# Kernel optimization log

Measured on AMD Instinct MI355X. Metric: run time of the kernel, lower is better.

Reference implementation:

```python
import jax, jax.numpy as jnp
import numpy as np

N = 100000   # nodes
E = 1600000  # edges
D = 128      # feature dim (layers all 128)
G = 512      # graphs in batch
C = 10       # num_classes
EPS = 1e-5   # batchnorm eps


def setup_inputs() -> dict:
    key = jax.random.key(0)
    ks = jax.random.split(key, 16)
    s = 1.0 / np.sqrt(D)
    return {
        "x": jax.random.normal(ks[0], (N, D), jnp.float32),
        "edge_index": jax.random.randint(ks[1], (2, E), 0, N),
        "batch": jnp.sort(jax.random.randint(ks[2], (N,), 0, G)),
        "w1": jax.random.normal(ks[3], (D, D), jnp.float32) * s,
        "b1": jnp.zeros((D,), jnp.float32),
        "w2": jax.random.normal(ks[4], (D, D), jnp.float32) * s,
        "b2": jnp.zeros((D,), jnp.float32),
        "w3": jax.random.normal(ks[5], (D, D), jnp.float32) * s,
        "b3": jnp.zeros((D,), jnp.float32),
        "g1": jnp.ones((D,), jnp.float32),
        "be1": jnp.zeros((D,), jnp.float32),
        "g2": jnp.ones((D,), jnp.float32),
        "be2": jnp.zeros((D,), jnp.float32),
        "fc_w": jax.random.normal(ks[6], (D, C), jnp.float32) * s,
        "fc_b": jnp.zeros((C,), jnp.float32),
    }


def _gcn(x, src, dst, norm, W, b):
    # transform -> gather -> normalize -> scatter-add (PyG GCNConv)
    h = x @ W
    out = jax.ops.segment_sum(h[src] * norm[:, None], dst, num_segments=x.shape[0])
    return out + b


def _bn(x, g, b):
    # training-mode BatchNorm1d: batch mean / biased variance
    mu = jnp.mean(x, axis=0)
    var = jnp.mean((x - mu) ** 2, axis=0)
    return (x - mu) * jax.lax.rsqrt(var + EPS) * g + b


def reference(x, edge_index, batch, w1, b1, w2, b2, w3, b3, g1, be1, g2, be2, fc_w, fc_b):
    n = x.shape[0]
    loop = jnp.arange(n)
    src = jnp.concatenate([edge_index[0], loop])  # add self-loops
    dst = jnp.concatenate([edge_index[1], loop])
    deg = jax.ops.segment_sum(jnp.ones_like(src, x.dtype), dst, num_segments=n)
    dinv = jax.lax.rsqrt(jnp.maximum(deg, 1.0))  # deg >= 1 due to self-loops
    norm = dinv[src] * dinv[dst]  # symmetric normalization per edge

    h = jax.nn.relu(_gcn(x, src, dst, norm, w1, b1))        # conv1 + relu (bn1 unused, per source)
    h = jax.nn.relu(_gcn(h, src, dst, norm, w2, b2))        # conv2 + relu
    h = jax.nn.relu(_bn(h, g1, be1))                        # bn + relu
    h = jax.nn.relu(_gcn(h, src, dst, norm, w3, b3))        # conv3 + relu
    h = jax.nn.relu(_bn(h, g2, be2))                        # bn + relu

    cnt = jax.ops.segment_sum(jnp.ones((n,), h.dtype), batch, num_segments=G)
    pooled = jax.ops.segment_sum(h, batch, num_segments=G) / jnp.maximum(cnt, 1.0)[:, None]
    logits = pooled @ fc_w + fc_b
    return jax.nn.log_softmax(logits, axis=1)
```

## Files before the change

### kernel.cpp

```cpp
#include <hip/hip_runtime.h>
#include <hip/hip_bf16.h>
#include <math.h>

#define D 128
#define G_GRAPHS 512
#define C_CLASSES 10
#define BN_EPS 1e-5f
#define NBUCK_MAX 512
#define EDGE_CHUNK 4096
#define EPT 16
#define HIST_BLOCKS 512
#define BN_BLOCKS 512

typedef unsigned short u16;
typedef unsigned int u32;
typedef unsigned short ushort4_t __attribute__((ext_vector_type(4)));
typedef unsigned short ushort8_t __attribute__((ext_vector_type(8)));
typedef __bf16 bf16x8 __attribute__((ext_vector_type(8)));
typedef float floatx4 __attribute__((ext_vector_type(4)));
union B8 { ushort8_t u; bf16x8 b; };

__device__ __forceinline__ float bf_lo(u32 v) { return __uint_as_float(v << 16); }
__device__ __forceinline__ float bf_hi(u32 v) { return __uint_as_float(v & 0xffff0000u); }
__device__ __forceinline__ u16 f2bf(float f) {
    union { float f; u32 u; } x; x.f = f;
    u32 r = x.u + 0x7fff + ((x.u >> 16) & 1);
    return (u16)(r >> 16);
}
__device__ __forceinline__ u32 pack2bf(float a, float b) {
    return (u32)f2bf(a) | ((u32)f2bf(b) << 16);
}


__global__ __launch_bounds__(256) void bucket_hist_kernel(
    const int* __restrict__ dst, int* __restrict__ bucketCnt, int E, int nbuck,
    const int* __restrict__ batch, int* __restrict__ gstart, int N)
{
    int tid = threadIdx.x;
    if (blockIdx.x >= HIST_BLOCKS) {
        int i = (blockIdx.x - HIST_BLOCKS) * 256 + tid;
        if (i >= N) return;
        int b = batch[i];
        int prev = (i == 0) ? -1 : batch[i - 1];
        if (b != prev) {
            for (int g = prev + 1; g <= b; ++g) gstart[g] = i;
        }
        if (i == N - 1) {
            for (int g = b + 1; g <= G_GRAPHS; ++g) gstart[g] = N;
        }
        return;
    }
    __shared__ int h[NBUCK_MAX];
    for (int i = tid; i < NBUCK_MAX; i += 256) h[i] = 0;
    __syncthreads();
    for (int i = blockIdx.x * 256 + tid; i < E; i += HIST_BLOCKS * 256)
        atomicAdd(&h[dst[i] >> 8], 1);
    __syncthreads();
    for (int i = tid; i < nbuck; i += 256)
        if (h[i]) atomicAdd(&bucketCnt[i], h[i]);
}

__global__ void scan_buckets_kernel(
    const int* __restrict__ bucketCnt, int* __restrict__ bucketBase,
    int* __restrict__ bucketCursor, int* __restrict__ rowPtr, int nbuck, int N, int E)
{
    __shared__ int buf[2][512];
    int tid = threadIdx.x;
    int v = (tid < nbuck) ? bucketCnt[tid] : 0;
    buf[0][tid] = v;
    __syncthreads();
    int cur = 0;
    for (int off = 1; off < 512; off <<= 1) {
        buf[1 - cur][tid] = buf[cur][tid] + ((tid >= off) ? buf[cur][tid - off] : 0);
        cur ^= 1;
        __syncthreads();
    }
    if (tid < nbuck) {
        int b = buf[cur][tid] - v;
        bucketBase[tid] = b;
        bucketCursor[tid] = b;
    }
    if (tid == 0) { bucketBase[nbuck] = E; rowPtr[N] = E; }
}

__global__ __launch_bounds__(256) void scatter_pairs_kernel(
    const int* __restrict__ src, const int* __restrict__ dst,
    int* __restrict__ bucketCursor, u32* __restrict__ pairs, int E)
{
    __shared__ int h[NBUCK_MAX];
    __shared__ int base[NBUCK_MAX];
    int tid = threadIdx.x;
    int e0 = blockIdx.x * EDGE_CHUNK;
    for (int i = tid; i < NBUCK_MAX; i += 256) h[i] = 0;
    __syncthreads();
    int s[EPT], d[EPT], r[EPT];
#pragma unroll
    for (int j = 0; j < EPT; ++j) {
        int i = e0 + j * 256 + tid;
        if (i < E) {
            s[j] = src[i];
            d[j] = dst[i];
            r[j] = atomicAdd(&h[d[j] >> 8], 1);
        } else {
            d[j] = -1;
        }
    }
    __syncthreads();
    for (int i = tid; i < NBUCK_MAX; i += 256)
        if (h[i]) base[i] = atomicAdd(&bucketCursor[i], h[i]);
    __syncthreads();
#pragma unroll
    for (int j = 0; j < EPT; ++j) {
        if (d[j] >= 0) {
            int b = d[j] >> 8;
            pairs[base[b] + r[j]] = ((u32)s[j] << 8) | (u32)(d[j] & 255);
        }
    }
}

__global__ __launch_bounds__(256) void bucket_sort_kernel(
    const u32* __restrict__ pairs, const int* __restrict__ bucketBase,
    int* __restrict__ colIdx, int* __restrict__ rowPtr, float* __restrict__ dinv,
    int* __restrict__ degHist, int N)
{
    __shared__ int h[256];
    __shared__ int cur[256];
    __shared__ int sbuf[2][256];
    __shared__ int dh[16];
    int tid = threadIdx.x;
    int b = blockIdx.x;
    int s = bucketBase[b], e = bucketBase[b + 1];
    h[tid] = 0;
    if (tid < 16) dh[tid] = 0;
    __syncthreads();
    for (int i = s + tid; i < e; i += 256)
        atomicAdd(&h[pairs[i] & 255], 1);
    __syncthreads();
    int cnt = h[tid];
    sbuf[0][tid] = cnt;
    __syncthreads();
    int c = 0;
    for (int off = 1; off < 256; off <<= 1) {
        sbuf[1 - c][tid] = sbuf[c][tid] + ((tid >= off) ? sbuf[c][tid - off] : 0);
        c ^= 1;
        __syncthreads();
    }
    int excl = sbuf[c][tid] - cnt;
    int v = b * 256 + tid;
    if (v < N) {
        rowPtr[v] = s + excl;
        dinv[v] = rsqrtf((float)(cnt + 1));
        int key = (cnt + 15) >> 4;
        if (key > 15) key = 15;
        atomicAdd(&dh[key], 1);
    }
    cur[tid] = s + excl;
    __syncthreads();
    if (tid < 16 && dh[tid]) atomicAdd(&degHist[tid * 16], dh[tid]);
    for (int i = s + tid; i < e; i += 256) {
        u32 p = pairs[i];
        int pos = atomicAdd(&cur[p & 255], 1);
        colIdx[pos] = (int)(p >> 8);
    }
}

__global__ __launch_bounds__(256) void wconv_kernel(
    const float4* __restrict__ w1, const float4* __restrict__ w2,
    const float4* __restrict__ w3, u16* __restrict__ wtAll, u32* __restrict__ tzero,
    const int* __restrict__ degHist, int* __restrict__ degCursor)
{
    int tid = threadIdx.x;
    if (blockIdx.x == 3) {
        if (tid < 64) tzero[tid] = 0;
        return;
    }
    if (blockIdx.x == 4) {
        if (tid == 0) {
            int base = 0;
            for (int k = 15; k >= 0; --k) {
                degCursor[k * 16] = base;
                base += degHist[k * 16];
            }
        }
        return;
    }
    const float4* W = (blockIdx.x == 0) ? w1 : (blockIdx.x == 1) ? w2 : w3;
    u16* Wt = wtAll + (size_t)blockIdx.x * D * D;
#pragma unroll
    for (int i = 0; i < 16; ++i) {
        int idx = tid + i * 256;
        int k = idx >> 5, c4 = idx & 31;
        float4 v = W[idx];
        Wt[(4 * c4 + 0) * D + k] = f2bf(v.x);
        Wt[(4 * c4 + 1) * D + k] = f2bf(v.y);
        Wt[(4 * c4 + 2) * D + k] = f2bf(v.z);
        Wt[(4 * c4 + 3) * D + k] = f2bf(v.w);
    }
}

__global__ __launch_bounds__(256) void perm_scatter_kernel(
    const int* __restrict__ rowPtr, int* __restrict__ degCursor,
    int* __restrict__ perm, int N)
{
    __shared__ int lh[16], lbase[16];
    int tid = threadIdx.x;
    if (tid < 16) lh[tid] = 0;
    __syncthreads();
    int v = blockIdx.x * 256 + tid;
    int key = 0, r = 0;
    bool ok = (v < N);
    if (ok) {
        int deg = rowPtr[v + 1] - rowPtr[v];
        key = (deg + 15) >> 4;
        if (key > 15) key = 15;
        r = atomicAdd(&lh[key], 1);
    }
    __syncthreads();
    if (tid < 16 && lh[tid] > 0) lbase[tid] = atomicAdd(&degCursor[tid * 16], lh[tid]);
    __syncthreads();
    if (ok) perm[lbase[key] + r] = v;
}

#define XS_STRIDE 136
#define GEMM_GRID 768

__device__ __forceinline__ void gemm_core_and_store(
    const u16* Xs, const u16* Ws, const float* __restrict__ dinv,
    u16* __restrict__ Y, int row0, int nrows, int tid)
{
    int wid = tid >> 6, lane = tid & 63;
    int m = lane & 15, quad = lane >> 4;
    int xrow = wid * 16 + m;

    floatx4 acc[8] = {};
#pragma unroll
    for (int ks = 0; ks < 4; ++ks) {
        int kk = ks * 32 + quad * 8;
        B8 a;
        a.u = *(const ushort8_t*)&Xs[xrow * XS_STRIDE + kk];
#pragma unroll
        for (int t = 0; t < 8; ++t) {
            B8 b;
            b.u = *(const ushort8_t*)&Ws[(t * 16 + m) * XS_STRIDE + kk];
            acc[t] = __builtin_amdgcn_mfma_f32_16x16x32_bf16(b.b, a.b, acc[t], 0, 0, 0);
        }
    }
    int grow = row0 + xrow;
    if (grow < nrows) {
        float du = dinv[grow];
#pragma unroll
        for (int t = 0; t < 8; ++t) {
            ushort4_t o;
            o.x = f2bf(acc[t][0] * du); o.y = f2bf(acc[t][1] * du);
            o.z = f2bf(acc[t][2] * du); o.w = f2bf(acc[t][3] * du);
            *(ushort4_t*)&Y[(size_t)grow * D + t * 16 + quad * 4] = o;
        }
    }
}

__device__ __forceinline__ void stage_w(const u16* __restrict__ Wt, u16* Ws, int tid) {
    const ushort8_t* Wv = (const ushort8_t*)Wt;
#pragma unroll
    for (int i = 0; i < 8; ++i) {
        int idx = tid + i * 256;
        int n = idx >> 4, c8 = idx & 15;
        *(ushort8_t*)&Ws[n * XS_STRIDE + c8 * 8] = Wv[idx];
    }
}

__global__ __launch_bounds__(256) void gemm_mfma_f32in_kernel(
    const float4* __restrict__ X, const u16* __restrict__ Wt,
    const float* __restrict__ dinv, u16* __restrict__ Y, int nrows, int ntiles)
{
    __shared__ __align__(16) u16 Xs[64 * XS_STRIDE];
    __shared__ __align__(16) u16 Ws[128 * XS_STRIDE];
    int tid = threadIdx.x;
    stage_w(Wt, Ws, tid);
    for (int t = blockIdx.x; t < ntiles; t += gridDim.x) {
        int row0 = t * 64;
        __syncthreads();
#pragma unroll
        for (int i = 0; i < 8; ++i) {
            int idx = tid + i * 256;
            int r = idx >> 5, c4 = idx & 31;
            int gr = row0 + r;
            float4 v = make_float4(0.f, 0.f, 0.f, 0.f);
            if (gr < nrows) v = X[(size_t)gr * 32 + c4];
            ushort4_t o;
            o.x = f2bf(v.x); o.y = f2bf(v.y); o.z = f2bf(v.z); o.w = f2bf(v.w);
            *(ushort4_t*)&Xs[r * XS_STRIDE + c4 * 4] = o;
        }
        __syncthreads();
        gemm_core_and_store(Xs, Ws, dinv, Y, row0, nrows, tid);
    }
}

__global__ __launch_bounds__(256) void gemm_mfma_bf16in_kernel(
    const uint4* __restrict__ X, const u16* __restrict__ Wt,
    const float* __restrict__ gsum, const float* __restrict__ gsq,
    const float* __restrict__ gamma, const float* __restrict__ beta, float invN,
    const float* __restrict__ dinv, u16* __restrict__ Y, int nrows, int ntiles)
{
    __shared__ __align__(16) u16 Xs[64 * XS_STRIDE];
    __shared__ __align__(16) u16 Ws[128 * XS_STRIDE];
    __shared__ float scs[D], shs[D];
    int tid = threadIdx.x;
    bool fuse = (gsum != nullptr);
    stage_w(Wt, Ws, tid);
    if (fuse && tid < D) {
        float mu = gsum[tid] * invN;
        float var = gsq[tid] * invN - mu * mu;
        float sc = gamma[tid] * rsqrtf(var + BN_EPS);
        scs[tid] = sc;
        shs[tid] = beta[tid] - mu * sc;
    }
    for (int t = blockIdx.x; t < ntiles; t += gridDim.x) {
        int row0 = t * 64;
        __syncthreads();
#pragma unroll
        for (int i = 0; i < 4; ++i) {
            int idx = tid + i * 256;
            int r = idx >> 4, c8 = idx & 15;
            int gr = row0 + r;
            uint4 v = make_uint4(0, 0, 0, 0);
            if (gr < nrows) v = X[(size_t)gr * 16 + c8];
            if (fuse) {
                int k = c8 * 8;
                v.x = pack2bf(fmaxf(bf_lo(v.x) * scs[k]     + shs[k],     0.f),
                              fmaxf(bf_hi(v.x) * scs[k + 1] + shs[k + 1], 0.f));
                v.y = pack2bf(fmaxf(bf_lo(v.y) * scs[k + 2] + shs[k + 2], 0.f),
                              fmaxf(bf_hi(v.y) * scs[k + 3] + shs[k + 3], 0.f));
                v.z = pack2bf(fmaxf(bf_lo(v.z) * scs[k + 4] + shs[k + 4], 0.f),
                              fmaxf(bf_hi(v.z) * scs[k + 5] + shs[k + 5], 0.f));
                v.w = pack2bf(fmaxf(bf_lo(v.w) * scs[k + 6] + shs[k + 6], 0.f),
                              fmaxf(bf_hi(v.w) * scs[k + 7] + shs[k + 7], 0.f));
            }
            *(uint4*)&Xs[r * XS_STRIDE + c8 * 8] = v;
        }
        __syncthreads();
        gemm_core_and_store(Xs, Ws, dinv, Y, row0, nrows, tid);
    }
}

#define ACC8U(t)                                           \
    acc0 += bf_lo((t).x); acc1 += bf_hi((t).x);            \
    acc2 += bf_lo((t).y); acc3 += bf_hi((t).y);            \
    acc4 += bf_lo((t).z); acc5 += bf_hi((t).z);            \
    acc6 += bf_lo((t).w); acc7 += bf_hi((t).w);

#define IDX8(i, jj)                                        \
    i##0 = ci[(jj)];     i##1 = ci[(jj) + 1];              \
    i##2 = ci[(jj) + 2]; i##3 = ci[(jj) + 3];              \
    i##4 = ci[(jj) + 4]; i##5 = ci[(jj) + 5];              \
    i##6 = ci[(jj) + 6]; i##7 = ci[(jj) + 7];

#define OFF8(o, i, jj)                                     \
    o##0 = ((jj)     < len) ? ((u32)i##0 << 8) : zoff;     \
    o##1 = ((jj) + 1 < len) ? ((u32)i##1 << 8) : zoff;     \
    o##2 = ((jj) + 2 < len) ? ((u32)i##2 << 8) : zoff;     \
    o##3 = ((jj) + 3 < len) ? ((u32)i##3 << 8) : zoff;     \
    o##4 = ((jj) + 4 < len) ? ((u32)i##4 << 8) : zoff;     \
    o##5 = ((jj) + 5 < len) ? ((u32)i##5 << 8) : zoff;     \
    o##6 = ((jj) + 6 < len) ? ((u32)i##6 << 8) : zoff;     \
    o##7 = ((jj) + 7 < len) ? ((u32)i##7 << 8) : zoff;

#define GAT8(t, o)                                         \
    t##0 = *(const uint4*)(baseT + o##0);                  \
    t##1 = *(const uint4*)(baseT + o##1);                  \
    t##2 = *(const uint4*)(baseT + o##2);                  \
    t##3 = *(const uint4*)(baseT + o##3);                  \
    t##4 = *(const uint4*)(baseT + o##4);                  \
    t##5 = *(const uint4*)(baseT + o##5);                  \
    t##6 = *(const uint4*)(baseT + o##6);                  \
    t##7 = *(const uint4*)(baseT + o##7);

#define ACCC(t)                                            \
    ACC8U(t##0); ACC8U(t##1); ACC8U(t##2); ACC8U(t##3);    \
    ACC8U(t##4); ACC8U(t##5); ACC8U(t##6); ACC8U(t##7);

__global__ __launch_bounds__(256) void aggregate_kernel(
    const uint4* __restrict__ T, const int* __restrict__ colIdx,
    const int* __restrict__ rowPtr, const float* __restrict__ dinv,
    const float* __restrict__ bias, const int* __restrict__ perm,
    u32* __restrict__ outH, int n, u32 zoff)
{
    int tid = threadIdx.x;
    int fg = tid & 15;
    int grp = tid >> 4;
    int slot = blockIdx.x * 16 + grp;
    if (slot >= n) return;
    int row = perm[slot];

    const char* baseT = (const char*)T + fg * 16;

    uint4 sv = *(const uint4*)(baseT + ((size_t)(u32)row << 8));
    float acc0 = bf_lo(sv.x), acc1 = bf_hi(sv.x);
    float acc2 = bf_lo(sv.y), acc3 = bf_hi(sv.y);
    float acc4 = bf_lo(sv.z), acc5 = bf_hi(sv.z);
    float acc6 = bf_lo(sv.w), acc7 = bf_hi(sv.w);

    int s = rowPtr[row], e = rowPtr[row + 1];
    int len = e - s;
    const int* ci = colIdx + s;

    if (len > 0) {
        int npairs = (len + 15) >> 4;
        int ia0, ia1, ia2, ia3, ia4, ia5, ia6, ia7;
        int ib0, ib1, ib2, ib3, ib4, ib5, ib6, ib7;
        u32 oa0, oa1, oa2, oa3, oa4, oa5, oa6, oa7;
        u32 ob0, ob1, ob2, ob3, ob4, ob5, ob6, ob7;
        uint4 t0, t1, t2, t3, t4, t5, t6, t7;
        uint4 u0, u1, u2, u3, u4, u5, u6, u7;

        IDX8(ia, 0); IDX8(ib, 8);
        OFF8(oa, ia, 0);
        GAT8(t, oa);
        OFF8(ob, ib, 8);
        IDX8(ia, 16);
        GAT8(u, ob);

#pragma unroll 1
        for (int p = 1; p < npairs; ++p) {
            int j = p << 4;
            OFF8(oa, ia, j);
            IDX8(ib, j + 8);
            ACCC(t);
            GAT8(t, oa);
            OFF8(ob, ib, j + 8);
            ACCC(u);
            IDX8(ia, j + 16);
            GAT8(u, ob);
        }
        ACCC(t); ACCC(u);
    }

    float dr = dinv[row];
    const float2* bp = (const float2*)bias;
    float2 bq0 = bp[fg * 4 + 0];
    float2 bq1 = bp[fg * 4 + 1];
    float2 bq2 = bp[fg * 4 + 2];
    float2 bq3 = bp[fg * 4 + 3];
    uint4 o;
    o.x = pack2bf(fmaxf(dr * acc0 + bq0.x, 0.f), fmaxf(dr * acc1 + bq0.y, 0.f));
    o.y = pack2bf(fmaxf(dr * acc2 + bq1.x, 0.f), fmaxf(dr * acc3 + bq1.y, 0.f));
    o.z = pack2bf(fmaxf(dr * acc4 + bq2.x, 0.f), fmaxf(dr * acc5 + bq2.y, 0.f));
    o.w = pack2bf(fmaxf(dr * acc6 + bq3.x, 0.f), fmaxf(dr * acc7 + bq3.y, 0.f));
    *(uint4*)&outH[(size_t)row * 64 + fg * 4] = o;
}

__global__ __launch_bounds__(256) void bn_stats_kernel(
    const uint4* __restrict__ H4, int n, float* __restrict__ partials,
    int* __restrict__ ticket, float* __restrict__ gsum, float* __restrict__ gsq)
{
    int tid = threadIdx.x;
    int fg = tid & 15;
    int grp = tid >> 4;
    float s0 = 0.f, s1 = 0.f, s2 = 0.f, s3 = 0.f, s4 = 0.f, s5 = 0.f, s6 = 0.f, s7 = 0.f;
    float q0 = 0.f, q1 = 0.f, q2 = 0.f, q3 = 0.f, q4 = 0.f, q5 = 0.f, q6 = 0.f, q7 = 0.f;
    for (int row = blockIdx.x * 16 + grp; row < n; row += BN_BLOCKS * 16) {
        uint4 v = H4[(size_t)row * 16 + fg];
        float a;
        a = bf_lo(v.x); s0 += a; q0 += a * a;
        a = bf_hi(v.x); s1 += a; q1 += a * a;
        a = bf_lo(v.y); s2 += a; q2 += a * a;
        a = bf_hi(v.y); s3 += a; q3 += a * a;
        a = bf_lo(v.z); s4 += a; q4 += a * a;
        a = bf_hi(v.z); s5 += a; q5 += a * a;
        a = bf_lo(v.w); s6 += a; q6 += a * a;
        a = bf_hi(v.w); s7 += a; q7 += a * a;
    }
    __shared__ float lsum[16][136];
    __shared__ float lsq[16][136];
    int ch = fg * 8;
    lsum[grp][ch + 0] = s0; lsum[grp][ch + 1] = s1; lsum[grp][ch + 2] = s2; lsum[grp][ch + 3] = s3;
    lsum[grp][ch + 4] = s4; lsum[grp][ch + 5] = s5; lsum[grp][ch + 6] = s6; lsum[grp][ch + 7] = s7;
    lsq[grp][ch + 0] = q0; lsq[grp][ch + 1] = q1; lsq[grp][ch + 2] = q2; lsq[grp][ch + 3] = q3;
    lsq[grp][ch + 4] = q4; lsq[grp][ch + 5] = q5; lsq[grp][ch + 6] = q6; lsq[grp][ch + 7] = q7;
    __syncthreads();
    if (tid < 128) {
        float s = 0.f;
#pragma unroll
        for (int g2 = 0; g2 < 16; ++g2) s += lsum[g2][tid];
        partials[(size_t)blockIdx.x * 256 + tid] = s;
    } else {
        int c2 = tid - 128;
        float q = 0.f;
#pragma unroll
        for (int g2 = 0; g2 < 16; ++g2) q += lsq[g2][c2];
        partials[(size_t)blockIdx.x * 256 + tid] = q;
    }
    __threadfence();
    __shared__ int lastFlag;
    if (tid == 0) lastFlag = (atomicAdd(ticket, 1) == BN_BLOCKS - 1);
    __syncthreads();
    if (!lastFlag) return;
    __threadfence();
    int g = tid >> 6;
    int j = (tid & 63) * 4;
    floatx4 a4 = {};
#pragma unroll 8
    for (int b = g; b < BN_BLOCKS; b += 4) {
        floatx4 v = *(const floatx4*)&partials[(size_t)b * 256 + j];
        a4 += v;
    }
    __shared__ floatx4 red[256];
    red[tid] = a4;
    __syncthreads();
    if (tid < 64) {
        floatx4 r = red[tid] + red[tid + 64] + red[tid + 128] + red[tid + 192];
#pragma unroll
        for (int k = 0; k < 4; ++k) {
            int p2 = 4 * tid + k;
            if (p2 < 128) gsum[p2] = r[k];
            else          gsq[p2 - 128] = r[k];
        }
    }
}

__global__ __launch_bounds__(256) void pool_classify_kernel(
    const u32* __restrict__ H, const float* __restrict__ gsum, const float* __restrict__ gsq,
    const float* __restrict__ gamma, const float* __restrict__ beta, float invN,
    const int* __restrict__ gstart, const float* __restrict__ fcw,
    const float* __restrict__ fcb, float* __restrict__ out)
{
    int g = blockIdx.x;
    int tid = threadIdx.x;
    int c = tid & 63, q = tid >> 6;
    float muA = gsum[2 * c] * invN, muB = gsum[2 * c + 1] * invN;
    float vA = gsq[2 * c] * invN - muA * muA, vB = gsq[2 * c + 1] * invN - muB * muB;
    float scA = gamma[2 * c] * rsqrtf(vA + BN_EPS), scB = gamma[2 * c + 1] * rsqrtf(vB + BN_EPS);
    float shA = beta[2 * c] - muA * scA, shB = beta[2 * c + 1] - muB * scB;

    int s = gstart[g], cnt = gstart[g + 1] - s;
    float aA = 0.f, aB = 0.f;
    for (int i = q; i < cnt; i += 4) {
        u32 v = H[(size_t)(s + i) * 64 + c];
        aA += fmaxf(bf_lo(v) * scA + shA, 0.f);
        aB += fmaxf(bf_hi(v) * scB + shB, 0.f);
    }
    __shared__ float sA[256], sB[256];
    __shared__ float prow[D];
    __shared__ float lg[C_CLASSES];
    sA[tid] = aA; sB[tid] = aB;
    __syncthreads();
    if (tid < 64) {
        float tA = sA[tid] + sA[tid + 64] + sA[tid + 128] + sA[tid + 192];
        float tB = sB[tid] + sB[tid + 64] + sB[tid + 128] + sB[tid + 192];
        float inv = 1.f / (float)(cnt > 1 ? cnt : 1);
        prow[2 * tid] = tA * inv;
        prow[2 * tid + 1] = tB * inv;
    }
    __syncthreads();
    if (tid < C_CLASSES) {
        float sum = fcb[tid];
        for (int d = 0; d < D; ++d) sum += prow[d] * fcw[d * C_CLASSES + tid];
        lg[tid] = sum;
    }
    __syncthreads();
    if (tid == 0) {
        float mx = -1e30f;
        for (int k = 0; k < C_CLASSES; ++k) mx = fmaxf(mx, lg[k]);
        float se = 0.f;
        for (int k = 0; k < C_CLASSES; ++k) se += expf(lg[k] - mx);
        float lse = mx + logf(se);
        for (int k = 0; k < C_CLASSES; ++k) out[(size_t)g * C_CLASSES + k] = lg[k] - lse;
    }
}

extern "C" void kernel_launch(void* const* d_in, const int* in_sizes, int n_in,
                              void* d_out, int out_size, void* d_ws, size_t ws_size,
                              hipStream_t stream) {
    const float* x   = (const float*)d_in[0];
    const int* ei    = (const int*)d_in[1];
    const int* batch = (const int*)d_in[2];
    const float* w1  = (const float*)d_in[3];
    const float* b1  = (const float*)d_in[4];
    const float* w2  = (const float*)d_in[5];
    const float* b2  = (const float*)d_in[6];
    const float* w3  = (const float*)d_in[7];
    const float* b3  = (const float*)d_in[8];
    const float* g1  = (const float*)d_in[9];
    const float* be1 = (const float*)d_in[10];
    const float* g2  = (const float*)d_in[11];
    const float* be2 = (const float*)d_in[12];
    const float* fcw = (const float*)d_in[13];
    const float* fcb = (const float*)d_in[14];

    const int N = in_sizes[0] / D;
    const int E = in_sizes[1] / 2;
    const int* src = ei;
    const int* dst = ei + E;
    const int nbuck = (N + 255) >> 8;
    const float invN = 1.f / (float)N;

    char* p = (char*)d_ws;
    auto alloc = [&](size_t bytes) -> void* {
        void* r = (void*)p;
        p += (bytes + 255) & ~(size_t)255;
        return r;
    };
    int*   bucketCnt    = (int*)alloc(NBUCK_MAX * 4);
    float* statsacc     = (float*)alloc(4 * D * 4);
    float* gsum1 = statsacc, *gsq1 = statsacc + D, *gsum2 = statsacc + 2 * D, *gsq2 = statsacc + 3 * D;
    int*   degHist      = (int*)alloc(2 * 16 * 16 * 4);
    int*   degCursor    = degHist + 256;
    int*   bnTick       = (int*)alloc(256);
    float* dinv     = (float*)alloc((size_t)N * 4);
    int*   rowPtr   = (int*)alloc((size_t)(N + 1) * 4);
    int*   colIdx   = (int*)alloc((size_t)E * 4);
    u32*   pairs    = (u32*)alloc((size_t)E * 4);
    int*   bucketBase   = (int*)alloc((NBUCK_MAX + 1) * 4);
    int*   bucketCursor = (int*)alloc(NBUCK_MAX * 4);
    int*   gstart  = (int*)alloc((G_GRAPHS + 1) * 4);
    int*   perm    = (int*)alloc((size_t)N * 4);
    float* bnPart  = (float*)alloc((size_t)BN_BLOCKS * 256 * 4);
    u16*   wtAll   = (u16*)alloc((size_t)3 * D * D * 2);
    u16*   tmp     = (u16*)alloc((size_t)(N + 1) * D * 2);
    u16*   hbuf    = (u16*)alloc((size_t)N * D * 2);

    hipMemsetAsync(bucketCnt, 0, NBUCK_MAX * 4 + 4 * D * 4 + 2 * 16 * 16 * 4 + 256, stream);

    bucket_hist_kernel<<<HIST_BLOCKS + (N + 255) / 256, 256, 0, stream>>>(
        dst, bucketCnt, E, nbuck, batch, gstart, N);
    scan_buckets_kernel<<<1, 512, 0, stream>>>(bucketCnt, bucketBase, bucketCursor, rowPtr, nbuck, N, E);
    scatter_pairs_kernel<<<(E + EDGE_CHUNK - 1) / EDGE_CHUNK, 256, 0, stream>>>(src, dst, bucketCursor, pairs, E);
    bucket_sort_kernel<<<nbuck, 256, 0, stream>>>(pairs, bucketBase, colIdx, rowPtr, dinv, degHist, N);
    wconv_kernel<<<5, 256, 0, stream>>>((const float4*)w1, (const float4*)w2, (const float4*)w3,
                                        wtAll, (u32*)(tmp + (size_t)N * D), degHist, degCursor);
    perm_scatter_kernel<<<(N + 255) / 256, 256, 0, stream>>>(rowPtr, degCursor, perm, N);

    const int NT = (N + 63) / 64;
    const int GB = NT < GEMM_GRID ? NT : GEMM_GRID;
    const int AB = (N + 15) / 16;
    const u32 ZOFF = (u32)N << 8;

    gemm_mfma_f32in_kernel<<<GB, 256, 0, stream>>>((const float4*)x, wtAll, dinv, tmp, N, NT);
    aggregate_kernel<<<AB, 256, 0, stream>>>((const uint4*)tmp, colIdx, rowPtr, dinv, b1, perm, (u32*)hbuf, N, ZOFF);
    gemm_mfma_bf16in_kernel<<<GB, 256, 0, stream>>>((const uint4*)hbuf, wtAll + D * D,
        nullptr, nullptr, nullptr, nullptr, 0.f, dinv, tmp, N, NT);
    aggregate_kernel<<<AB, 256, 0, stream>>>((const uint4*)tmp, colIdx, rowPtr, dinv, b2, perm, (u32*)hbuf, N, ZOFF);
    bn_stats_kernel<<<BN_BLOCKS, 256, 0, stream>>>((const uint4*)hbuf, N, bnPart, bnTick, gsum1, gsq1);
    gemm_mfma_bf16in_kernel<<<GB, 256, 0, stream>>>((const uint4*)hbuf, wtAll + 2 * D * D,
        gsum1, gsq1, g1, be1, invN, dinv, tmp, N, NT);
    aggregate_kernel<<<AB, 256, 0, stream>>>((const uint4*)tmp, colIdx, rowPtr, dinv, b3, perm, (u32*)hbuf, N, ZOFF);
    bn_stats_kernel<<<BN_BLOCKS, 256, 0, stream>>>((const uint4*)hbuf, N, bnPart, bnTick + 16, gsum2, gsq2);
    pool_classify_kernel<<<G_GRAPHS, 256, 0, stream>>>((const u32*)hbuf, gsum2, gsq2, g2, be2, invN,
        gstart, fcw, fcb, (float*)d_out);
}
```

Baseline: 524.3 us.

## Split transformed features into 16-column slabs for cache-local gather aggregation

The GEMM output is stored as eight column slabs of 16 bf16 values (32 bytes per row), each with its own zero row, instead of one row-major 256-byte row per node. The aggregate kernel now assigns blocks to a single slab, with two threads per destination row reading 16-byte halves. Each gather pass then works over a 3.2 MB slab, which should stay resident in L2/LLC and cut the cost of the random neighbour reads. The trade-off is that every edge's colIdx is re-read eight times, and gathers become 32-byte segments instead of full 256-byte rows.

```diff
diff --git a/kernel.cpp b/kernel.cpp
--- a/kernel.cpp
+++ b/kernel.cpp
@@ -166,12 +166,15 @@
 
 __global__ __launch_bounds__(256) void wconv_kernel(
     const float4* __restrict__ w1, const float4* __restrict__ w2,
-    const float4* __restrict__ w3, u16* __restrict__ wtAll, u32* __restrict__ tzero,
-    const int* __restrict__ degHist, int* __restrict__ degCursor)
+    const float4* __restrict__ w3, u16* __restrict__ wtAll, u32* __restrict__ tbase,
+    const int* __restrict__ degHist, int* __restrict__ degCursor, int N)
 {
     int tid = threadIdx.x;
     if (blockIdx.x == 3) {
-        if (tid < 64) tzero[tid] = 0;
+        if (tid < 64) {
+            int slab = tid >> 3, word = tid & 7;
+            tbase[((size_t)slab * (N + 1) + N) * 8 + word] = 0;
+        }
         return;
     }
     if (blockIdx.x == 4) {
@@ -226,7 +229,7 @@
 
 __device__ __forceinline__ void gemm_core_and_store(
     const u16* Xs, const u16* Ws, const float* __restrict__ dinv,
-    u16* __restrict__ Y, int row0, int nrows, int tid)
+    u16* __restrict__ Y, int slabStride16, int row0, int nrows, int tid)
 {
     int wid = tid >> 6, lane = tid & 63;
     int m = lane & 15, quad = lane >> 4;
@@ -253,7 +256,7 @@
             ushort4_t o;
             o.x = f2bf(acc[t][0] * du); o.y = f2bf(acc[t][1] * du);
             o.z = f2bf(acc[t][2] * du); o.w = f2bf(acc[t][3] * du);
-            *(ushort4_t*)&Y[(size_t)grow * D + t * 16 + quad * 4] = o;
+            *(ushort4_t*)&Y[(size_t)t * slabStride16 + (size_t)grow * 16 + quad * 4] = o;
         }
     }
 }
@@ -270,7 +273,8 @@
 
 __global__ __launch_bounds__(256) void gemm_mfma_f32in_kernel(
     const float4* __restrict__ X, const u16* __restrict__ Wt,
-    const float* __restrict__ dinv, u16* __restrict__ Y, int nrows, int ntiles)
+    const float* __restrict__ dinv, u16* __restrict__ Y, int slabStride16,
+    int nrows, int ntiles)
 {
     __shared__ __align__(16) u16 Xs[64 * XS_STRIDE];
     __shared__ __align__(16) u16 Ws[128 * XS_STRIDE];
@@ -291,7 +295,7 @@
             *(ushort4_t*)&Xs[r * XS_STRIDE + c4 * 4] = o;
         }
         __syncthreads();
-        gemm_core_and_store(Xs, Ws, dinv, Y, row0, nrows, tid);
+        gemm_core_and_store(Xs, Ws, dinv, Y, slabStride16, row0, nrows, tid);
     }
 }
 
@@ -299,7 +303,8 @@
     const uint4* __restrict__ X, const u16* __restrict__ Wt,
     const float* __restrict__ gsum, const float* __restrict__ gsq,
     const float* __restrict__ gamma, const float* __restrict__ beta, float invN,
-    const float* __restrict__ dinv, u16* __restrict__ Y, int nrows, int ntiles)
+    const float* __restrict__ dinv, u16* __restrict__ Y, int slabStride16,
+    int nrows, int ntiles)
 {
     __shared__ __align__(16) u16 Xs[64 * XS_STRIDE];
     __shared__ __align__(16) u16 Ws[128 * XS_STRIDE];
@@ -338,7 +343,7 @@
             *(uint4*)&Xs[r * XS_STRIDE + c8 * 8] = v;
         }
         __syncthreads();
-        gemm_core_and_store(Xs, Ws, dinv, Y, row0, nrows, tid);
+        gemm_core_and_store(Xs, Ws, dinv, Y, slabStride16, row0, nrows, tid);
     }
 }
 
@@ -355,14 +360,14 @@
     i##6 = ci[(jj) + 6]; i##7 = ci[(jj) + 7];
 
 #define OFF8(o, i, jj)                                     \
-    o##0 = ((jj)     < len) ? ((u32)i##0 << 8) : zoff;     \
-    o##1 = ((jj) + 1 < len) ? ((u32)i##1 << 8) : zoff;     \
-    o##2 = ((jj) + 2 < len) ? ((u32)i##2 << 8) : zoff;     \
-    o##3 = ((jj) + 3 < len) ? ((u32)i##3 << 8) : zoff;     \
-    o##4 = ((jj) + 4 < len) ? ((u32)i##4 << 8) : zoff;     \
-    o##5 = ((jj) + 5 < len) ? ((u32)i##5 << 8) : zoff;     \
-    o##6 = ((jj) + 6 < len) ? ((u32)i##6 << 8) : zoff;     \
-    o##7 = ((jj) + 7 < len) ? ((u32)i##7 << 8) : zoff;
+    o##0 = ((jj)     < len) ? ((u32)i##0 << 5) : zoff;     \
+    o##1 = ((jj) + 1 < len) ? ((u32)i##1 << 5) : zoff;     \
+    o##2 = ((jj) + 2 < len) ? ((u32)i##2 << 5) : zoff;     \
+    o##3 = ((jj) + 3 < len) ? ((u32)i##3 << 5) : zoff;     \
+    o##4 = ((jj) + 4 < len) ? ((u32)i##4 << 5) : zoff;     \
+    o##5 = ((jj) + 5 < len) ? ((u32)i##5 << 5) : zoff;     \
+    o##6 = ((jj) + 6 < len) ? ((u32)i##6 << 5) : zoff;     \
+    o##7 = ((jj) + 7 < len) ? ((u32)i##7 << 5) : zoff;
 
 #define GAT8(t, o)                                         \
     t##0 = *(const uint4*)(baseT + o##0);                  \
@@ -379,21 +384,24 @@
     ACC8U(t##4); ACC8U(t##5); ACC8U(t##6); ACC8U(t##7);
 
 __global__ __launch_bounds__(256) void aggregate_kernel(
-    const uint4* __restrict__ T, const int* __restrict__ colIdx,
+    const char* __restrict__ T, const int* __restrict__ colIdx,
     const int* __restrict__ rowPtr, const float* __restrict__ dinv,
     const float* __restrict__ bias, const int* __restrict__ perm,
-    u32* __restrict__ outH, int n, u32 zoff)
-{
-    int tid = threadIdx.x;
-    int fg = tid & 15;
-    int grp = tid >> 4;
-    int slot = blockIdx.x * 16 + grp;
+    u32* __restrict__ outH, int n, int nplus1)
+{
+    int tid = threadIdx.x;
+    int sl = blockIdx.x & 7;
+    int chunk = blockIdx.x >> 3;
+    int rl = tid >> 1;
+    int h = tid & 1;
+    int slot = chunk * 128 + rl;
     if (slot >= n) return;
     int row = perm[slot];
 
-    const char* baseT = (const char*)T + fg * 16;
-
-    uint4 sv = *(const uint4*)(baseT + ((size_t)(u32)row << 8));
+    const char* baseT = T + (size_t)sl * nplus1 * 32 + h * 16;
+    u32 zoff = (u32)n << 5;
+
+    uint4 sv = *(const uint4*)(baseT + ((u32)row << 5));
     float acc0 = bf_lo(sv.x), acc1 = bf_hi(sv.x);
     float acc2 = bf_lo(sv.y), acc3 = bf_hi(sv.y);
     float acc4 = bf_lo(sv.z), acc5 = bf_hi(sv.z);
@@ -436,16 +444,16 @@
 
     float dr = dinv[row];
     const float2* bp = (const float2*)bias;
-    float2 bq0 = bp[fg * 4 + 0];
-    float2 bq1 = bp[fg * 4 + 1];
-    float2 bq2 = bp[fg * 4 + 2];
-    float2 bq3 = bp[fg * 4 + 3];
+    float2 bq0 = bp[sl * 8 + h * 4 + 0];
+    float2 bq1 = bp[sl * 8 + h * 4 + 1];
+    float2 bq2 = bp[sl * 8 + h * 4 + 2];
+    float2 bq3 = bp[sl * 8 + h * 4 + 3];
     uint4 o;
     o.x = pack2bf(fmaxf(dr * acc0 + bq0.x, 0.f), fmaxf(dr * acc1 + bq0.y, 0.f));
     o.y = pack2bf(fmaxf(dr * acc2 + bq1.x, 0.f), fmaxf(dr * acc3 + bq1.y, 0.f));
     o.z = pack2bf(fmaxf(dr * acc4 + bq2.x, 0.f), fmaxf(dr * acc5 + bq2.y, 0.f));
     o.w = pack2bf(fmaxf(dr * acc6 + bq3.x, 0.f), fmaxf(dr * acc7 + bq3.y, 0.f));
-    *(uint4*)&outH[(size_t)row * 64 + fg * 4] = o;
+    *(uint4*)&outH[(size_t)row * 64 + sl * 8 + h * 4] = o;
 }
 
 __global__ __launch_bounds__(256) void bn_stats_kernel(
@@ -592,6 +600,8 @@
     const int* dst = ei + E;
     const int nbuck = (N + 255) >> 8;
     const float invN = 1.f / (float)N;
+    const int NP1 = N + 1;
+    const int SLAB16 = NP1 * 16;
 
     char* p = (char*)d_ws;
     auto alloc = [&](size_t bytes) -> void* {
@@ -615,7 +625,7 @@
     int*   perm    = (int*)alloc((size_t)N * 4);
     float* bnPart  = (float*)alloc((size_t)BN_BLOCKS * 256 * 4);
     u16*   wtAll   = (u16*)alloc((size_t)3 * D * D * 2);
-    u16*   tmp     = (u16*)alloc((size_t)(N + 1) * D * 2);
+    u16*   tmp     = (u16*)alloc((size_t)8 * SLAB16 * 2);
     u16*   hbuf    = (u16*)alloc((size_t)N * D * 2);
 
     hipMemsetAsync(bucketCnt, 0, NBUCK_MAX * 4 + 4 * D * 4 + 2 * 16 * 16 * 4 + 256, stream);
@@ -626,23 +636,22 @@
     scatter_pairs_kernel<<<(E + EDGE_CHUNK - 1) / EDGE_CHUNK, 256, 0, stream>>>(src, dst, bucketCursor, pairs, E);
     bucket_sort_kernel<<<nbuck, 256, 0, stream>>>(pairs, bucketBase, colIdx, rowPtr, dinv, degHist, N);
     wconv_kernel<<<5, 256, 0, stream>>>((const float4*)w1, (const float4*)w2, (const float4*)w3,
-                                        wtAll, (u32*)(tmp + (size_t)N * D), degHist, degCursor);
+                                        wtAll, (u32*)tmp, degHist, degCursor, N);
     perm_scatter_kernel<<<(N + 255) / 256, 256, 0, stream>>>(rowPtr, degCursor, perm, N);
 
     const int NT = (N + 63) / 64;
     const int GB = NT < GEMM_GRID ? NT : GEMM_GRID;
-    const int AB = (N + 15) / 16;
-    const u32 ZOFF = (u32)N << 8;
-
-    gemm_mfma_f32in_kernel<<<GB, 256, 0, stream>>>((const float4*)x, wtAll, dinv, tmp, N, NT);
-    aggregate_kernel<<<AB, 256, 0, stream>>>((const uint4*)tmp, colIdx, rowPtr, dinv, b1, perm, (u32*)hbuf, N, ZOFF);
+    const int AB = 8 * ((N + 127) / 128);
+
+    gemm_mfma_f32in_kernel<<<GB, 256, 0, stream>>>((const float4*)x, wtAll, dinv, tmp, SLAB16, N, NT);
+    aggregate_kernel<<<AB, 256, 0, stream>>>((const char*)tmp, colIdx, rowPtr, dinv, b1, perm, (u32*)hbuf, N, NP1);
     gemm_mfma_bf16in_kernel<<<GB, 256, 0, stream>>>((const uint4*)hbuf, wtAll + D * D,
-        nullptr, nullptr, nullptr, nullptr, 0.f, dinv, tmp, N, NT);
-    aggregate_kernel<<<AB, 256, 0, stream>>>((const uint4*)tmp, colIdx, rowPtr, dinv, b2, perm, (u32*)hbuf, N, ZOFF);
+        nullptr, nullptr, nullptr, nullptr, 0.f, dinv, tmp, SLAB16, N, NT);
+    aggregate_kernel<<<AB, 256, 0, stream>>>((const char*)tmp, colIdx, rowPtr, dinv, b2, perm, (u32*)hbuf, N, NP1);
     bn_stats_kernel<<<BN_BLOCKS, 256, 0, stream>>>((const uint4*)hbuf, N, bnPart, bnTick, gsum1, gsq1);
     gemm_mfma_bf16in_kernel<<<GB, 256, 0, stream>>>((const uint4*)hbuf, wtAll + 2 * D * D,
-        gsum1, gsq1, g1, be1, invN, dinv, tmp, N, NT);
-    aggregate_kernel<<<AB, 256, 0, stream>>>((const uint4*)tmp, colIdx, rowPtr, dinv, b3, perm, (u32*)hbuf, N, ZOFF);
+        gsum1, gsq1, g1, be1, invN, dinv, tmp, SLAB16, N, NT);
+    aggregate_kernel<<<AB, 256, 0, stream>>>((const char*)tmp, colIdx, rowPtr, dinv, b3, perm, (u32*)hbuf, N, NP1);
     bn_stats_kernel<<<BN_BLOCKS, 256, 0, stream>>>((const uint4*)hbuf, N, bnPart, bnTick + 16, gsum2, gsq2);
     pool_classify_kernel<<<G_GRAPHS, 256, 0, stream>>>((const u32*)hbuf, gsum2, gsq2, g2, be2, invN,
         gstart, fcw, fcb, (float*)d_out);
```

Measured after the change: 599.6 us. +14.4%, slower.
